# Kernel optimization log

Measured on AMD Instinct MI355X. Metric: run time of the kernel, lower is better.

## Reference

```python
import jax, jax.numpy as jnp
import numpy as np

B, C, H, W = 4, 192, 56, 56


def setup_inputs() -> dict:
    key = jax.random.key(0)
    k1, k2, k3 = jax.random.split(key, 3)
    x = jax.random.normal(k1, (B, C, H, W), dtype=jnp.float32)
    conv_w = jax.random.normal(k2, (C, 2 * C), dtype=jnp.float32) * (1.0 / np.sqrt(2 * C))
    conv_b = jax.random.normal(k3, (C,), dtype=jnp.float32) * 0.01
    bn_gamma = jnp.ones((C,), dtype=jnp.float32)
    bn_beta = jnp.zeros((C,), dtype=jnp.float32)
    bn_mean = jnp.zeros((C,), dtype=jnp.float32)
    bn_var = jnp.ones((C,), dtype=jnp.float32)
    return {"x": x, "conv_w": conv_w, "conv_b": conv_b, "bn_gamma": bn_gamma,
            "bn_beta": bn_beta, "bn_mean": bn_mean, "bn_var": bn_var, "K": 4}


def reference(x, conv_w, conv_b, bn_gamma, bn_beta, bn_mean, bn_var, K):
    b, c, h, w = x.shape
    shifts_h = list(range(0, h, K))          # rolls along H
    shifts_w = list(range(K, w, K))          # rolls along W
    n = len(shifts_h) + len(shifts_w)
    scale = n ** (-0.5)
    # (B, n, C, H, W): all circularly shifted copies (static shift set)
    rolled = jnp.stack([jnp.roll(x, i, axis=2) for i in shifts_h] +
                       [jnp.roll(x, j, axis=3) for j in shifts_w], axis=1)
    # scores: tanh(scale * x * x_rolled), summed over channels -> (B, n, 1, H, W)
    scores = jnp.tanh(rolled * x[:, None] * scale).sum(axis=2, keepdims=True)
    weights = jax.nn.softmax(scores, axis=1)
    out = (rolled * weights).sum(axis=1)     # (B, C, H, W)
    cat = jnp.concatenate([x, out], axis=1)  # (B, 2C, H, W)
    # 1x1 conv as GEMM over channels
    y = jnp.einsum('bchw,oc->bohw', cat, conv_w) + conv_b[None, :, None, None]
    # BatchNorm2d in eval mode (running stats)
    eps = 1e-5
    inv = bn_gamma / jnp.sqrt(bn_var + eps)
    y = (y - bn_mean[None, :, None, None]) * inv[None, :, None, None] + bn_beta[None, :, None, None]
    return jax.nn.gelu(y, approximate=False)
```

## Files before the change

### kernel.cpp

```cpp
#include <hip/hip_runtime.h>
#include <hip/hip_bf16.h>
#include <hip/hip_fp16.h>
#include <math.h>

#define BB 4
#define CC 192
#define HH 56
#define WW 56
#define HWW 3136

typedef __attribute__((ext_vector_type(8))) short short8;
typedef __attribute__((ext_vector_type(4))) short short4v;
typedef __attribute__((ext_vector_type(8))) _Float16 half8;
typedef __attribute__((ext_vector_type(4))) float f32x4;

__device__ __forceinline__ unsigned short f2b(float f) {
    __hip_bfloat16 h = __float2bfloat16(f);
    return __builtin_bit_cast(unsigned short, h);
}
__device__ __forceinline__ float b2f(unsigned short u) {
    unsigned int x = ((unsigned int)u) << 16;
    return __builtin_bit_cast(float, x);
}
__device__ __forceinline__ unsigned short f2h(float f) {
    __half h = __float2half_rn(f);
    return __builtin_bit_cast(unsigned short, h);
}
__device__ __forceinline__ float2 h2f2(unsigned int u) {
    return __half22float2(__builtin_bit_cast(__half2, u));
}

__global__ __launch_bounds__(256) void k_pre(const float* __restrict__ x,
                                             const float* __restrict__ cw,
                                             unsigned short* __restrict__ xth,
                                             unsigned short* __restrict__ xtl,
                                             unsigned short* __restrict__ xh16,
                                             unsigned short* __restrict__ wh16) {
    int tid = threadIdx.x, bid = blockIdx.x;
    if (bid < 2352) {
        __shared__ float tile[32][33];
        int b = bid / 588, rem = bid % 588;
        int by = rem / 98, bx = rem % 98;
        int tx = tid & 31, ty = tid >> 5;
        int p0 = bx * 32, c0 = by * 32;
#pragma unroll
        for (int i = 0; i < 4; i++) {
            int c = c0 + ty + 8 * i;
            tile[ty + 8 * i][tx] = x[(b * CC + c) * HWW + p0 + tx];
        }
        __syncthreads();
#pragma unroll
        for (int i = 0; i < 4; i++) {
            int p = p0 + ty + 8 * i;
            float v = tile[tx][ty + 8 * i];
            unsigned short hi = f2b(v);
            size_t o = (size_t)(b * HWW + p) * CC + c0 + tx;
            xth[o] = hi;
            xtl[o] = f2b(v - b2f(hi));
            xh16[o] = f2h(v);
        }
    } else {
        int i = (bid - 2352) * 256 + tid;
        if (i < 384 * 192) {
            int n = i / 192, k = i % 192;
            float v = (n < 192) ? cw[n * 384 + k] : cw[(n - 192) * 384 + 192 + k];
            wh16[i] = f2h(v);
        }
    }
}

__global__ __launch_bounds__(256) void k_mid(const unsigned short* __restrict__ xth,
                                             const unsigned short* __restrict__ xtl,
                                             const unsigned short* __restrict__ xh16,
                                             const unsigned short* __restrict__ wh16,
                                             float* __restrict__ sp,
                                             float* __restrict__ u,
                                             float* __restrict__ z) {
    __shared__ __align__(16) char smem[18432];
    int tid = threadIdx.x, bid = blockIdx.x;

    if (bid < 1792) {
        float* Xs = (float*)smem;
        const float K2 = 0.38490017945975050f;
        bool isH = bid < 896;
        int lid = isH ? bid : bid - 896;
        int half = lid & 1;
        int rp = (lid >> 1) & 1;
        int cb2 = lid >> 2;
        int b = cb2 / 56, l0 = cb2 % 56;
        int r0 = rp * 2;

        const unsigned short* srch = xth + (size_t)(b * HWW) * CC + half * 96;
        const unsigned short* srcl = xtl + (size_t)(b * HWW) * CC + half * 96;
        for (int idx = tid; idx < 28 * 12; idx += 256) {
            int t2 = idx / 12, cq = idx % 12;
            int pi = (r0 + t2 / 14) + 4 * (t2 % 14);
            int pix = isH ? (pi * WW + l0) : (l0 * WW + pi);
            short8 h8 = *(const short8*)(srch + (size_t)pix * CC + cq * 8);
            short8 l8 = *(const short8*)(srcl + (size_t)pix * CC + cq * 8);
            float o[8];
#pragma unroll
            for (int e = 0; e < 8; e++)
                o[e] = b2f((unsigned short)h8[e]) + b2f((unsigned short)l8[e]);
            *(float4*)&Xs[t2 * 100 + cq * 8] = *(float4*)&o[0];
            *(float4*)&Xs[t2 * 100 + cq * 8 + 4] = *(float4*)&o[4];
        }
        __syncthreads();

        int perCls = isH ? 105 : 91;
        if (tid < 2 * perCls) {
            int cls = tid / perCls, p = tid % perCls;
            int a, bb;
            if (isH) {
                a = (int)((sqrtf((float)(8 * p + 1)) - 1.0f) * 0.5f);
                bb = p - (a * (a + 1)) / 2;
            } else {
                int ap = (int)((sqrtf((float)(8 * p + 1)) - 1.0f) * 0.5f);
                bb = p - (ap * (ap + 1)) / 2;
                a = ap + 1;
            }
            const float* pA = &Xs[(cls * 14 + a) * 100];
            const float* pB = &Xs[(cls * 14 + bb) * 100];
            float s0 = 0.f, s1 = 0.f, s2 = 0.f, s3 = 0.f;
#pragma unroll
            for (int q = 0; q < 24; q++) {
                float4 av = *(const float4*)(pA + q * 4);
                float4 bv = *(const float4*)(pB + q * 4);
                s0 += __builtin_amdgcn_rcpf(__expf(av.x * bv.x * K2) + 1.0f);
                s1 += __builtin_amdgcn_rcpf(__expf(av.y * bv.y * K2) + 1.0f);
                s2 += __builtin_amdgcn_rcpf(__expf(av.z * bv.z * K2) + 1.0f);
                s3 += __builtin_amdgcn_rcpf(__expf(av.w * bv.w * K2) + 1.0f);
            }
            float s = 96.0f - 2.0f * (s0 + s1 + s2 + s3);
            int r = r0 + cls;
            size_t base = (size_t)(half * BB + b) * HWW;
            if (isH) {
                int i1 = a - bb;
                int h1 = r + 4 * a, h2 = r + 4 * bb;
                sp[(base + h1 * WW + l0) * 32 + i1] = s;
                if (a != bb) sp[(base + h2 * WW + l0) * 32 + (14 - i1)] = s;
            } else {
                int d = a - bb;
                int w1 = r + 4 * a, w2 = r + 4 * bb;
                sp[(base + l0 * WW + w1) * 32 + 14 + (d - 1)] = s;
                sp[(base + l0 * WW + w2) * 32 + 14 + (13 - d)] = s;
            }
        }
        return;
    }

    {
        unsigned short* Ah = (unsigned short*)smem;
        unsigned short* Bh = Ah + 64 * 72;
        float* Ds = (float*)smem;
        int vb = bid - 1792;
        int bm = (vb % 196) * 64, bn = (vb / 196) * 64;
        int lane = tid & 63, wv = tid >> 6;

        f32x4 acc[4] = {{0,0,0,0},{0,0,0,0},{0,0,0,0},{0,0,0,0}};

        for (int kc = 0; kc < 3; kc++) {
#pragma unroll
            for (int r2 = 0; r2 < 2; r2++) {
                int idx = tid + r2 * 256;
                int m = idx >> 3, kq = idx & 7;
                size_t ao = (size_t)(bm + m) * CC + kc * 64 + kq * 8;
                *(short8*)&Ah[m * 72 + kq * 8] = *(const short8*)(xh16 + ao);
                size_t bo = (size_t)(bn + m) * 192 + kc * 64 + kq * 8;
                *(short8*)&Bh[m * 72 + kq * 8] = *(const short8*)(wh16 + bo);
            }
            __syncthreads();
            int n0 = wv * 16;
            int k8 = lane >> 4;
            int col = lane & 15;
#pragma unroll
            for (int ks = 0; ks < 64; ks += 32) {
                int koff = ks + k8 * 8;
                half8 bf = *(const half8*)&Bh[(n0 + col) * 72 + koff];
#pragma unroll
                for (int fm = 0; fm < 4; fm++) {
                    half8 af = *(const half8*)&Ah[(fm * 16 + col) * 72 + koff];
                    acc[fm] = __builtin_amdgcn_mfma_f32_16x16x32_f16(af, bf, acc[fm], 0, 0, 0);
                }
            }
            __syncthreads();
        }
        {
            int col = lane & 15, rowq = lane >> 4;
#pragma unroll
            for (int fm = 0; fm < 4; fm++)
#pragma unroll
                for (int rg = 0; rg < 4; rg++)
                    Ds[(fm * 16 + rowq * 4 + rg) * 68 + wv * 16 + col] = acc[fm][rg];
        }
        __syncthreads();
        {
            int c4 = tid & 15, m0 = tid >> 4;
            int cg = bn + c4 * 4;
            float* dst = (cg < 192) ? u : z;
            int cc = (cg < 192) ? cg : cg - 192;
#pragma unroll
            for (int p = 0; p < 4; p++) {
                int m = m0 + p * 16;
                float4 v = *(float4*)&Ds[m * 68 + c4 * 4];
                *(float4*)&dst[(size_t)(bm + m) * CC + cc] = v;
            }
        }
    }
}

__global__ __launch_bounds__(448, 1) void k_tail(const float* __restrict__ u,
                                                 const float* __restrict__ z,
                                                 const float* __restrict__ sp,
                                                 const float* __restrict__ cb,
                                                 const float* __restrict__ gma,
                                                 const float* __restrict__ bta,
                                                 const float* __restrict__ mea,
                                                 const float* __restrict__ var,
                                                 float* __restrict__ y) {
    __shared__ float Zs[14 * 56 * 8];
    __shared__ __align__(16) unsigned short W16[392 * 36];
    int tid = threadIdx.x, bid = blockIdx.x;
    int th = bid & 1;
    int t1 = bid >> 1;
    int cc = t1 % 24;
    int t2 = t1 / 24;
    int r = t2 & 3;
    int b = t2 >> 2;
    int w = tid >> 3, c = tid & 7;
    int cg = cc * 8 + c;
    int hbase = r + 4 * (th * 7);

    float4 zva0, zva1, zvb0, zvb1;
    {
        int idx = tid;
        int t = idx / 56, ww = idx - t * 56;
        const float* s = z + ((size_t)(b * HWW + (r + 4 * t) * WW + ww)) * CC + cc * 8;
        zva0 = *(const float4*)s;
        zva1 = *(const float4*)(s + 4);
    }
    if (tid < 336) {
        int idx = tid + 448;
        int t = idx / 56, ww = idx - t * 56;
        const float* s = z + ((size_t)(b * HWW + (r + 4 * t) * WW + ww)) * CC + cc * 8;
        zvb0 = *(const float4*)s;
        zvb1 = *(const float4*)(s + 4);
    }

    if (tid < 392) {
        int tq = tid / 56, ww = tid - tq * 56;
        int row = hbase + 4 * tq;
        size_t gp = (size_t)b * HWW + row * WW + ww;
        const float4* p0 = (const float4*)&sp[gp * 32];
        const float4* p1 = (const float4*)&sp[((size_t)(4 * HWW) + gp) * 32];
        float sc[28];
#pragma unroll
        for (int j = 0; j < 7; j++) {
            float4 a4 = p0[j], v4 = p1[j];
            sc[4 * j + 0] = a4.x + v4.x; sc[4 * j + 1] = a4.y + v4.y;
            sc[4 * j + 2] = a4.z + v4.z; sc[4 * j + 3] = a4.w + v4.w;
        }
        float mx = -1e30f;
#pragma unroll
        for (int s = 0; s < 27; s++) mx = fmaxf(mx, sc[s]);
        float sum = 0.f;
#pragma unroll
        for (int s = 0; s < 27; s++) { sc[s] = __expf(sc[s] - mx); sum += sc[s]; }
        float inv = __builtin_amdgcn_rcpf(sum);
        unsigned short hw[28];
#pragma unroll
        for (int s = 0; s < 27; s++) hw[s] = f2h(sc[s] * inv);
        hw[27] = 0;
        unsigned short* d = &W16[tid * 36];
        *(short8*)(d)      = *(short8*)&hw[0];
        *(short8*)(d + 8)  = *(short8*)&hw[8];
        *(short8*)(d + 16) = *(short8*)&hw[16];
        *(short4v*)(d + 24) = *(short4v*)&hw[24];
    }

    {
        float* dst = &Zs[tid * 8];
        *(float4*)dst = zva0;
        *(float4*)(dst + 4) = zva1;
    }
    if (tid < 336) {
        float* dst = &Zs[(tid + 448) * 8];
        *(float4*)dst = zvb0;
        *(float4*)(dst + 4) = zvb1;
    }
    __syncthreads();

    float zc[14];
#pragma unroll
    for (int m = 0; m < 14; m++) {
        int t0 = m + th * 7;
        if (t0 >= 14) t0 -= 14;
        zc[m] = Zs[(t0 * 56 + w) * 8 + c];
    }

    float bias = cb[cg];
    float ginv = gma[cg] * rsqrtf(var[cg] + 1e-5f);
    float bt = bta[cg];
    float me = mea[cg];

    float acc0[7];
#pragma unroll
    for (int tt = 0; tt < 7; tt++) {
        int pix = (hbase + 4 * tt) * WW + w;
        acc0[tt] = u[((size_t)(b * HWW + pix)) * CC + cg];
    }

#pragma unroll
    for (int tt = 0; tt < 7; tt++) {
        int t = th * 7 + tt;
        int pix = (hbase + 4 * tt) * WW + w;
        int pb = (tt * 56 + w) * 36;
        float a = acc0[tt];

#pragma unroll
        for (int p = 0; p < 7; p++) {
            float2 f2 = h2f2(*(const unsigned int*)&W16[pb + 2 * p]);
            a += f2.x * zc[(tt - 2 * p + 28) % 14];
            a += f2.y * zc[(tt - 2 * p - 1 + 28) % 14];
        }
#pragma unroll
        for (int p = 7; p < 14; p++) {
            float2 f2 = h2f2(*(const unsigned int*)&W16[pb + 2 * p]);
            int j0 = 2 * p - 13, j1 = 2 * p - 12;
            int wj0 = w - 4 * j0; if (wj0 < 0) wj0 += 56;
            int wj1 = w - 4 * j1; if (wj1 < 0) wj1 += 56;
            a += f2.x * Zs[(t * 56 + wj0) * 8 + c];
            a += f2.y * Zs[(t * 56 + wj1) * 8 + c];
        }

        float v = (a + bias - me) * ginv + bt;
        v = 0.5f * v * (1.0f + erff(v * 0.70710678118654752f));
        y[((size_t)(b * CC + cg)) * HWW + pix] = v;
    }
}

extern "C" void kernel_launch(void* const* d_in, const int* in_sizes, int n_in,
                              void* d_out, int out_size, void* d_ws, size_t ws_size,
                              hipStream_t stream) {
    const float* x   = (const float*)d_in[0];
    const float* cw  = (const float*)d_in[1];
    const float* cb  = (const float*)d_in[2];
    const float* gma = (const float*)d_in[3];
    const float* bta = (const float*)d_in[4];
    const float* mea = (const float*)d_in[5];
    const float* var = (const float*)d_in[6];
    float* out = (float*)d_out;

    float* ws = (float*)d_ws;
    float*          sp   = ws;
    float*          u    = ws + 802816;
    float*          z    = ws + 3211264;
    unsigned short* xth  = (unsigned short*)(ws + 5619712);
    unsigned short* xtl  = (unsigned short*)(ws + 6823936);
    unsigned short* xh16 = (unsigned short*)(ws + 8028160);
    unsigned short* wh16 = (unsigned short*)(ws + 9232384);

    k_pre<<<2640, 256, 0, stream>>>(x, cw, xth, xtl, xh16, wh16);
    k_mid<<<2968, 256, 0, stream>>>(xth, xtl, xh16, wh16, sp, u, z);
    k_tail<<<768, 448, 0, stream>>>(u, z, sp, cb, gma, bta, mea, var, out);
}
```

Baseline: 125.8 us.

## Store GEMM outputs in tail-blocked layout and stage output through shared memory

```diff
diff --git a/kernel.cpp b/kernel.cpp
--- a/kernel.cpp
+++ b/kernel.cpp
@@ -199,11 +199,18 @@
             int cg = bn + c4 * 4;
             float* dst = (cg < 192) ? u : z;
             int cc = (cg < 192) ? cg : cg - 192;
+            int cc8 = cc >> 3, ci = cc & 7;
+            size_t cbase = (size_t)cc8 * 100352;
 #pragma unroll
             for (int p = 0; p < 4; p++) {
                 int m = m0 + p * 16;
+                int gp = bm + m;
+                int b = gp / HWW, pp = gp - b * HWW;
+                int hh = pp / 56, ww2 = pp - hh * 56;
+                int rr = hh & 3, tt2 = hh >> 2;
+                size_t off = cbase + ((size_t)((b * 4 + rr) * 14 + tt2)) * 448 + ww2 * 8 + ci;
                 float4 v = *(float4*)&Ds[m * 68 + c4 * 4];
-                *(float4*)&dst[(size_t)(bm + m) * CC + cc] = v;
+                *(float4*)&dst[off] = v;
             }
         }
     }
@@ -218,8 +225,11 @@
                                                  const float* __restrict__ mea,
                                                  const float* __restrict__ var,
                                                  float* __restrict__ y) {
-    __shared__ float Zs[14 * 56 * 8];
-    __shared__ __align__(16) unsigned short W16[392 * 36];
+    __shared__ __align__(16) char arena[25088 + 28224];
+    float* Zs = (float*)arena;
+    unsigned short* W16 = (unsigned short*)(arena + 25088);
+    float* Ys = (float*)(arena + 25088);
+
     int tid = threadIdx.x, bid = blockIdx.x;
     int th = bid & 1;
     int t1 = bid >> 1;
@@ -231,21 +241,21 @@
     int cg = cc * 8 + c;
     int hbase = r + 4 * (th * 7);
 
-    float4 zva0, zva1, zvb0, zvb1;
-    {
-        int idx = tid;
-        int t = idx / 56, ww = idx - t * 56;
-        const float* s = z + ((size_t)(b * HWW + (r + 4 * t) * WW + ww)) * CC + cc * 8;
-        zva0 = *(const float4*)s;
-        zva1 = *(const float4*)(s + 4);
-    }
+    size_t slab = ((size_t)cc * BB + b) * 4 + r;
+    const float* zg = z + slab * 6272;
+    const float* ug = u + slab * 6272;
+
+    float4 zva0 = *(const float4*)(zg + tid * 8);
+    float4 zva1 = *(const float4*)(zg + tid * 8 + 4);
+    float4 zvb0, zvb1;
     if (tid < 336) {
-        int idx = tid + 448;
-        int t = idx / 56, ww = idx - t * 56;
-        const float* s = z + ((size_t)(b * HWW + (r + 4 * t) * WW + ww)) * CC + cc * 8;
-        zvb0 = *(const float4*)s;
-        zvb1 = *(const float4*)(s + 4);
-    }
+        zvb0 = *(const float4*)(zg + (tid + 448) * 8);
+        zvb1 = *(const float4*)(zg + (tid + 448) * 8 + 4);
+    }
+    float acc0[7];
+#pragma unroll
+    for (int tt = 0; tt < 7; tt++)
+        acc0[tt] = ug[(th * 7 + tt) * 448 + tid];
 
     if (tid < 392) {
         int tq = tid / 56, ww = tid - tq * 56;
@@ -303,17 +313,10 @@
     float bt = bta[cg];
     float me = mea[cg];
 
-    float acc0[7];
-#pragma unroll
-    for (int tt = 0; tt < 7; tt++) {
-        int pix = (hbase + 4 * tt) * WW + w;
-        acc0[tt] = u[((size_t)(b * HWW + pix)) * CC + cg];
-    }
-
+    float vout[7];
 #pragma unroll
     for (int tt = 0; tt < 7; tt++) {
         int t = th * 7 + tt;
-        int pix = (hbase + 4 * tt) * WW + w;
         int pb = (tt * 56 + w) * 36;
         float a = acc0[tt];
 
@@ -334,8 +337,20 @@
         }
 
         float v = (a + bias - me) * ginv + bt;
-        v = 0.5f * v * (1.0f + erff(v * 0.70710678118654752f));
-        y[((size_t)(b * CC + cg)) * HWW + pix] = v;
+        vout[tt] = 0.5f * v * (1.0f + erff(v * 0.70710678118654752f));
+    }
+
+    __syncthreads();
+#pragma unroll
+    for (int tt = 0; tt < 7; tt++)
+        Ys[tt * 448 + c * 56 + w] = vout[tt];
+    __syncthreads();
+    {
+        int c_out = tid / 56, w_out = tid - c_out * 56;
+        size_t ybase = ((size_t)(b * CC + cc * 8 + c_out)) * HWW + w_out;
+#pragma unroll
+        for (int tt = 0; tt < 7; tt++)
+            y[ybase + (size_t)(hbase + 4 * tt) * 56] = Ys[tt * 448 + c_out * 56 + w_out];
     }
 }
 
```

Result: faster. 121.6 us (-3.4%).
